# Performance work log

Measured on AMD Instinct MI355X. Metric: run time of the kernel, lower is better.

The kernel has to match this reference:

```python
import jax, jax.numpy as jnp
import numpy as np

B = 16384        # batch
I = 35           # input_dim (number of metadata features)
E = 256          # embedding_dim
C = E // 4       # continuous_size = 64


def setup_inputs() -> dict:
    key = jax.random.key(0)
    ks = jax.random.split(key, 12)
    # metadata rows 0-2 are continuous (depth, coverage, read_length); row 3 is runtype in {-2,-1,0,1}
    cont = jax.random.normal(ks[0], (B, 3, I), dtype=jnp.float32)
    run = jax.random.randint(ks[1], (B, 1, I), -2, 2).astype(jnp.float32)
    metadata = jnp.concatenate([cont, run], axis=1)  # [B, 4, I]
    s = 0.05
    return {
        "metadata": metadata,
        # per-feature Linear(1, C): weight [I, C] (squeezed from (C,1)), bias [I, C]
        "Wd": jax.random.normal(ks[2], (I, C), jnp.float32) * s,
        "bd": jax.random.normal(ks[3], (I, C), jnp.float32) * s,
        "Wc": jax.random.normal(ks[4], (I, C), jnp.float32) * s,
        "bc": jax.random.normal(ks[5], (I, C), jnp.float32) * s,
        "Wr": jax.random.normal(ks[6], (I, C), jnp.float32) * s,
        "br": jax.random.normal(ks[7], (I, C), jnp.float32) * s,
        # per-feature Embedding(4, C): [I, 4, C]
        "emb": jax.random.normal(ks[8], (I, 4, C), jnp.float32) * s,
        # final Linear(I*4*C -> E), torch convention weight [out, in]
        "Wf": jax.random.normal(ks[9], (E, I * 4 * C), jnp.float32) * s,
        "bf": jax.random.normal(ks[10], (E,), jnp.float32) * s,
        # LayerNorm affine params
        "gamma": jnp.ones((E,), jnp.float32),
        "beta": jnp.zeros((E,), jnp.float32),
    }


def _layer_norm(x, gamma, beta, eps=1e-5):
    mu = jnp.mean(x, axis=-1, keepdims=True)
    var = jnp.var(x, axis=-1, keepdims=True)  # biased, matches torch LayerNorm
    return (x - mu) * jax.lax.rsqrt(var + eps) * gamma + beta


def reference(metadata, Wd, bd, Wc, bc, Wr, br, emb, Wf, bf, gamma, beta):
    depth = metadata[:, 0, :]   # [B, I]
    cov = metadata[:, 1, :]
    rlen = metadata[:, 2, :]
    rt = metadata[:, 3, :].astype(jnp.int32)  # [B, I]
    rt = jnp.where(rt == -1, 2, rt)
    rt = jnp.where(rt == -2, 3, rt)

    # fused per-feature Linear(1, C): scalar * weight + bias, broadcast over all features at once
    de = depth[:, :, None] * Wd[None] + bd[None]   # [B, I, C]
    ce = cov[:, :, None] * Wc[None] + bc[None]     # [B, I, C]
    re_ = rlen[:, :, None] * Wr[None] + br[None]   # [B, I, C]
    # per-feature embedding gather: emb[i, rt[b, i]] -> [B, I, C]
    rte = emb[jnp.arange(I)[None, :], rt]

    feat = jnp.concatenate([de, ce, re_, rte], axis=-1)  # [B, I, 4C]
    feat = feat.reshape(B, I * 4 * C)                    # [B, 8960]

    out = feat @ Wf.T + bf                               # [B, E]
    out = _layer_norm(out, gamma, beta)
    return jnp.maximum(out, 0.0)  # non_linearity=True -> ReLU
```

## Files before the change

kernel.cpp:

```cpp
#include <hip/hip_runtime.h>

#define B_    16384
#define I_    35
#define ISLOT 36
#define E_    256
#define KP    288
#define F_    140
#define MROWS 32
#define NBLK  (B_ / MROWS)
#define LROW  296

typedef short bf16x8 __attribute__((ext_vector_type(8)));
typedef float f32x4  __attribute__((ext_vector_type(4)));

__device__ __forceinline__ unsigned short f2bf(float f) {
    unsigned int u = __float_as_uint(f);
    u += 0x7FFFu + ((u >> 16) & 1u);
    return (unsigned short)(u >> 16);
}

__global__ __launch_bounds__(256) void precompute_kernel(
    const float* __restrict__ Wd, const float* __restrict__ bd,
    const float* __restrict__ Wc, const float* __restrict__ bc,
    const float* __restrict__ Wr, const float* __restrict__ br,
    const float* __restrict__ emb, const float* __restrict__ Wf,
    const float* __restrict__ bf,
    unsigned short* __restrict__ At, float* __restrict__ base)
{
    __shared__ float wfs[8960];
    __shared__ float dots[7][40];
    __shared__ float bds[3][40];
    const int e = blockIdx.x, t = threadIdx.x;

    const float4* src = (const float4*)(Wf + (size_t)e * 8960);
    float4* dst = (float4*)wfs;
    for (int idx = t; idx < 2240; idx += 256) dst[idx] = src[idx];
    __syncthreads();

    if (t < 245) {
        const int g = t / 35, i = t - 35 * g;
        const int gsel = (g < 3) ? g : 3;
        const float* wf = wfs + i * 256 + gsel * 64;
        const float* tab = (g == 0) ? (Wd + i * 64)
                         : (g == 1) ? (Wc + i * 64)
                         : (g == 2) ? (Wr + i * 64)
                         : (emb + ((size_t)i * 4 + (g - 3)) * 64);
        const float* btab = (g == 0) ? (bd + i * 64)
                          : (g == 1) ? (bc + i * 64) : (br + i * 64);
        float dot = 0.f, bdot = 0.f;
        #pragma unroll 16
        for (int cc = 0; cc < 64; ++cc) {
            const int c = (cc + t) & 63;
            const float wv = wf[c];
            dot = fmaf(tab[c], wv, dot);
            if (g < 3) bdot = fmaf(btab[c], wv, bdot);
        }
        dots[g][i] = dot;
        if (g < 3) bds[g][i] = bdot;
    }
    __syncthreads();

    if (t < ISLOT) {
        union { unsigned short h[8]; int4 v; } p;
        if (t < I_) {
            const float v0 = dots[3][t], v1 = dots[4][t], v2 = dots[5][t], v3 = dots[6][t];
            const float a = v1 - v0, b = v2 - v0, c = v3 - v0;
            const float k2 = 0.5f * (a + b);
            const float s  = 0.5f * (a - b);
            const float u  = 0.5f * (4.f * k2 - c);
            const float k3 = (u - s) * (1.f / 3.f);
            const float k1 = s - k3;
            p.h[0] = f2bf(dots[0][t]); p.h[1] = f2bf(dots[1][t]); p.h[2] = f2bf(dots[2][t]);
            p.h[3] = f2bf(k1);         p.h[4] = f2bf(k2);         p.h[5] = f2bf(k3);
            p.h[6] = 0; p.h[7] = 0;
        } else {
            p.v = make_int4(0, 0, 0, 0);
        }
        *(int4*)(At + (size_t)e * KP + t * 8) = p.v;
    }
    if (t < 64) {
        float part = (t < I_) ? (bds[0][t] + bds[1][t] + bds[2][t] + dots[3][t]) : 0.f;
        #pragma unroll
        for (int mm = 1; mm < 64; mm <<= 1) part += __shfl_xor(part, mm, 64);
        if (t == 0) base[e] = bf[e] + part;
    }
}

__global__ __launch_bounds__(256) void main_kernel(
    const float* __restrict__ metadata,
    const unsigned short* __restrict__ At,
    const float* __restrict__ base,
    const float* __restrict__ gamma, const float* __restrict__ beta,
    float* __restrict__ out)
{
    __shared__ unsigned short feat[MROWS * LROW];
    __shared__ float redS[4][MROWS];
    __shared__ float redQ[4][MROWS];

    const int t  = threadIdx.x;
    const int b0 = blockIdx.x * MROWS;

    const int lane = t & 63, w = t >> 6;
    const int nlo = lane & 15, q = lane >> 4;

    float baseN[4], gmN[4], btN[4];
    #pragma unroll
    for (int nn = 0; nn < 4; ++nn) {
        const int e = w * 64 + nn * 16 + nlo;
        baseN[nn] = base[e]; gmN[nn] = gamma[e]; btN[nn] = beta[e];
    }

    for (int cell = t; cell < MROWS * ISLOT; cell += 256) {
        const int r = cell / ISLOT, i = cell - r * ISLOT;
        union { unsigned short h[8]; int4 v; } p;
        if (i < I_) {
            const float* mp = metadata + (size_t)(b0 + r) * F_ + i;
            const float d = mp[0], c = mp[I_], rl = mp[2 * I_], x = mp[3 * I_];
            const float x2 = x * x, x3 = x2 * x;
            p.h[0] = f2bf(d);  p.h[1] = f2bf(c);  p.h[2] = f2bf(rl);
            p.h[3] = f2bf(x);  p.h[4] = f2bf(x2); p.h[5] = f2bf(x3);
            p.h[6] = 0; p.h[7] = 0;
        } else {
            p.v = make_int4(0, 0, 0, 0);
        }
        *(int4*)(feat + r * LROW + i * 8) = p.v;
    }
    __syncthreads();

    f32x4 acc[2][4];
    #pragma unroll
    for (int mt = 0; mt < 2; ++mt)
        #pragma unroll
        for (int nn = 0; nn < 4; ++nn) acc[mt][nn] = (f32x4){0.f, 0.f, 0.f, 0.f};

    const unsigned short* ga = feat + nlo * LROW + q * 8;
    const unsigned short* gb = At + ((size_t)(w * 64 + nlo)) * KP + q * 8;

    #pragma unroll 3
    for (int ks = 0; ks < KP / 32; ++ks) {
        const bf16x8 a0 = *(const bf16x8*)(ga + ks * 32);
        const bf16x8 a1 = *(const bf16x8*)(ga + 16 * LROW + ks * 32);
        #pragma unroll
        for (int nn = 0; nn < 4; ++nn) {
            const bf16x8 b = *(const bf16x8*)(gb + (size_t)nn * 16 * KP + ks * 32);
            acc[0][nn] = __builtin_amdgcn_mfma_f32_16x16x32_bf16(a0, b, acc[0][nn], 0, 0, 0);
            acc[1][nn] = __builtin_amdgcn_mfma_f32_16x16x32_bf16(a1, b, acc[1][nn], 0, 0, 0);
        }
    }

    #pragma unroll
    for (int mt = 0; mt < 2; ++mt) {
        #pragma unroll
        for (int reg = 0; reg < 4; ++reg) {
            float s = 0.f, qq = 0.f;
            #pragma unroll
            for (int nn = 0; nn < 4; ++nn) {
                const float v = acc[mt][nn][reg] + baseN[nn];
                acc[mt][nn][reg] = v;
                s += v; qq += v * v;
            }
            #pragma unroll
            for (int mm = 1; mm < 16; mm <<= 1) {
                s  += __shfl_xor(s, mm, 64);
                qq += __shfl_xor(qq, mm, 64);
            }
            if (nlo == 0) {
                const int row = mt * 16 + q * 4 + reg;
                redS[w][row] = s; redQ[w][row] = qq;
            }
        }
    }
    __syncthreads();

    #pragma unroll
    for (int mt = 0; mt < 2; ++mt) {
        #pragma unroll
        for (int reg = 0; reg < 4; ++reg) {
            const int row = mt * 16 + q * 4 + reg;
            const float S = redS[0][row] + redS[1][row] + redS[2][row] + redS[3][row];
            const float Q = redQ[0][row] + redQ[1][row] + redQ[2][row] + redQ[3][row];
            const float mu   = S * (1.f / E_);
            const float var  = Q * (1.f / E_) - mu * mu;
            const float rstd = rsqrtf(var + 1e-5f);
            float* orow = out + (size_t)(b0 + row) * E_ + w * 64 + nlo;
            #pragma unroll
            for (int nn = 0; nn < 4; ++nn) {
                const float v = (acc[mt][nn][reg] - mu) * rstd * gmN[nn] + btN[nn];
                orow[nn * 16] = fmaxf(v, 0.f);
            }
        }
    }
}

extern "C" void kernel_launch(void* const* d_in, const int* in_sizes, int n_in,
                              void* d_out, int out_size, void* d_ws, size_t ws_size,
                              hipStream_t stream) {
    const float* metadata = (const float*)d_in[0];
    const float* Wd  = (const float*)d_in[1];
    const float* bd  = (const float*)d_in[2];
    const float* Wc  = (const float*)d_in[3];
    const float* bc  = (const float*)d_in[4];
    const float* Wr  = (const float*)d_in[5];
    const float* br  = (const float*)d_in[6];
    const float* emb = (const float*)d_in[7];
    const float* Wf  = (const float*)d_in[8];
    const float* bf  = (const float*)d_in[9];
    const float* gamma = (const float*)d_in[10];
    const float* beta  = (const float*)d_in[11];

    unsigned short* At = (unsigned short*)d_ws;
    float* basep = (float*)((char*)d_ws + (size_t)E_ * KP * 2);

    precompute_kernel<<<E_, 256, 0, stream>>>(Wd, bd, Wc, bc, Wr, br, emb, Wf, bf,
                                              At, basep);
    main_kernel<<<NBLK, 256, 0, stream>>>(metadata, At, basep, gamma, beta,
                                          (float*)d_out);
}
```

Baseline: 123.6 us.

## Pack K dimension densely, permute output columns for float4 stores, parallelize precompute

Measured after the change: 106.9 us, median of 2. -13.5%, faster.

```diff
diff --git a/kernel.cpp b/kernel.cpp
--- a/kernel.cpp
+++ b/kernel.cpp
@@ -2,13 +2,12 @@
 
 #define B_    16384
 #define I_    35
-#define ISLOT 36
 #define E_    256
-#define KP    288
+#define KP    224
 #define F_    140
 #define MROWS 32
 #define NBLK  (B_ / MROWS)
-#define LROW  296
+#define LROW  232
 
 typedef short bf16x8 __attribute__((ext_vector_type(8)));
 typedef float f32x4  __attribute__((ext_vector_type(4)));
@@ -19,7 +18,7 @@
     return (unsigned short)(u >> 16);
 }
 
-__global__ __launch_bounds__(256) void precompute_kernel(
+__global__ __launch_bounds__(512) void precompute_kernel(
     const float* __restrict__ Wd, const float* __restrict__ bd,
     const float* __restrict__ Wc, const float* __restrict__ bc,
     const float* __restrict__ Wr, const float* __restrict__ br,
@@ -27,56 +26,74 @@
     const float* __restrict__ bf,
     unsigned short* __restrict__ At, float* __restrict__ base)
 {
-    __shared__ float wfs[8960];
     __shared__ float dots[7][40];
     __shared__ float bds[3][40];
     const int e = blockIdx.x, t = threadIdx.x;
-
-    const float4* src = (const float4*)(Wf + (size_t)e * 8960);
-    float4* dst = (float4*)wfs;
-    for (int idx = t; idx < 2240; idx += 256) dst[idx] = src[idx];
+    const int grp = t >> 4, gl = t & 15;
+
+    const float* wfrow = Wf + (size_t)e * 8960;
+
+    for (int u = grp; u < 140; u += 32) {
+        const int i = u >> 2, part = u & 3;
+        const float* wf = wfrow + i * 256 + part * 64;
+        float wv[4];
+        #pragma unroll
+        for (int j = 0; j < 4; ++j) wv[j] = wf[gl + 16 * j];
+        if (part < 3) {
+            const float* tab  = ((part == 0) ? Wd : (part == 1) ? Wc : Wr) + i * 64;
+            const float* btab = ((part == 0) ? bd : (part == 1) ? bc : br) + i * 64;
+            float dot = 0.f, bdot = 0.f;
+            #pragma unroll
+            for (int j = 0; j < 4; ++j) {
+                const int c = gl + 16 * j;
+                dot  = fmaf(tab[c],  wv[j], dot);
+                bdot = fmaf(btab[c], wv[j], bdot);
+            }
+            #pragma unroll
+            for (int mm = 1; mm < 16; mm <<= 1) {
+                dot  += __shfl_xor(dot,  mm, 64);
+                bdot += __shfl_xor(bdot, mm, 64);
+            }
+            if (gl == 0) { dots[part][i] = dot; bds[part][i] = bdot; }
+        } else {
+            const float* et = emb + (size_t)i * 256;
+            float d0 = 0.f, d1 = 0.f, d2 = 0.f, d3 = 0.f;
+            #pragma unroll
+            for (int j = 0; j < 4; ++j) {
+                const int c = gl + 16 * j;
+                d0 = fmaf(et[c],       wv[j], d0);
+                d1 = fmaf(et[64 + c],  wv[j], d1);
+                d2 = fmaf(et[128 + c], wv[j], d2);
+                d3 = fmaf(et[192 + c], wv[j], d3);
+            }
+            #pragma unroll
+            for (int mm = 1; mm < 16; mm <<= 1) {
+                d0 += __shfl_xor(d0, mm, 64);
+                d1 += __shfl_xor(d1, mm, 64);
+                d2 += __shfl_xor(d2, mm, 64);
+                d3 += __shfl_xor(d3, mm, 64);
+            }
+            if (gl == 0) { dots[3][i] = d0; dots[4][i] = d1; dots[5][i] = d2; dots[6][i] = d3; }
+        }
+    }
     __syncthreads();
 
-    if (t < 245) {
-        const int g = t / 35, i = t - 35 * g;
-        const int gsel = (g < 3) ? g : 3;
-        const float* wf = wfs + i * 256 + gsel * 64;
-        const float* tab = (g == 0) ? (Wd + i * 64)
-                         : (g == 1) ? (Wc + i * 64)
-                         : (g == 2) ? (Wr + i * 64)
-                         : (emb + ((size_t)i * 4 + (g - 3)) * 64);
-        const float* btab = (g == 0) ? (bd + i * 64)
-                          : (g == 1) ? (bc + i * 64) : (br + i * 64);
-        float dot = 0.f, bdot = 0.f;
-        #pragma unroll 16
-        for (int cc = 0; cc < 64; ++cc) {
-            const int c = (cc + t) & 63;
-            const float wv = wf[c];
-            dot = fmaf(tab[c], wv, dot);
-            if (g < 3) bdot = fmaf(btab[c], wv, bdot);
-        }
-        dots[g][i] = dot;
-        if (g < 3) bds[g][i] = bdot;
-    }
-    __syncthreads();
-
-    if (t < ISLOT) {
-        union { unsigned short h[8]; int4 v; } p;
-        if (t < I_) {
-            const float v0 = dots[3][t], v1 = dots[4][t], v2 = dots[5][t], v3 = dots[6][t];
-            const float a = v1 - v0, b = v2 - v0, c = v3 - v0;
-            const float k2 = 0.5f * (a + b);
-            const float s  = 0.5f * (a - b);
-            const float u  = 0.5f * (4.f * k2 - c);
-            const float k3 = (u - s) * (1.f / 3.f);
-            const float k1 = s - k3;
-            p.h[0] = f2bf(dots[0][t]); p.h[1] = f2bf(dots[1][t]); p.h[2] = f2bf(dots[2][t]);
-            p.h[3] = f2bf(k1);         p.h[4] = f2bf(k2);         p.h[5] = f2bf(k3);
-            p.h[6] = 0; p.h[7] = 0;
-        } else {
-            p.v = make_int4(0, 0, 0, 0);
-        }
-        *(int4*)(At + (size_t)e * KP + t * 8) = p.v;
+    const int v = (e & ~63) | ((e & 3) << 4) | ((e & 63) >> 2);
+
+    if (t < I_) {
+        const float v0 = dots[3][t], v1 = dots[4][t], v2 = dots[5][t], v3 = dots[6][t];
+        const float a = v1 - v0, b = v2 - v0, c = v3 - v0;
+        const float k2 = 0.5f * (a + b);
+        const float s  = 0.5f * (a - b);
+        const float uu = 0.5f * (4.f * k2 - c);
+        const float k3 = (uu - s) * (1.f / 3.f);
+        const float k1 = s - k3;
+        unsigned int* dst = (unsigned int*)(At + (size_t)v * KP + t * 6);
+        dst[0] = (unsigned int)f2bf(dots[0][t]) | ((unsigned int)f2bf(dots[1][t]) << 16);
+        dst[1] = (unsigned int)f2bf(dots[2][t]) | ((unsigned int)f2bf(k1) << 16);
+        dst[2] = (unsigned int)f2bf(k2)         | ((unsigned int)f2bf(k3) << 16);
+    } else if (t < I_ + 7) {
+        ((unsigned int*)(At + (size_t)v * KP))[105 + t - I_] = 0;
     }
     if (t < 64) {
         float part = (t < I_) ? (bds[0][t] + bds[1][t] + bds[2][t] + dots[3][t]) : 0.f;
@@ -103,27 +120,26 @@
     const int lane = t & 63, w = t >> 6;
     const int nlo = lane & 15, q = lane >> 4;
 
-    float baseN[4], gmN[4], btN[4];
-    #pragma unroll
-    for (int nn = 0; nn < 4; ++nn) {
-        const int e = w * 64 + nn * 16 + nlo;
-        baseN[nn] = base[e]; gmN[nn] = gamma[e]; btN[nn] = beta[e];
-    }
-
-    for (int cell = t; cell < MROWS * ISLOT; cell += 256) {
-        const int r = cell / ISLOT, i = cell - r * ISLOT;
-        union { unsigned short h[8]; int4 v; } p;
-        if (i < I_) {
-            const float* mp = metadata + (size_t)(b0 + r) * F_ + i;
-            const float d = mp[0], c = mp[I_], rl = mp[2 * I_], x = mp[3 * I_];
-            const float x2 = x * x, x3 = x2 * x;
-            p.h[0] = f2bf(d);  p.h[1] = f2bf(c);  p.h[2] = f2bf(rl);
-            p.h[3] = f2bf(x);  p.h[4] = f2bf(x2); p.h[5] = f2bf(x3);
-            p.h[6] = 0; p.h[7] = 0;
-        } else {
-            p.v = make_int4(0, 0, 0, 0);
-        }
-        *(int4*)(feat + r * LROW + i * 8) = p.v;
+    const float4 bs4 = *(const float4*)(base  + w * 64 + nlo * 4);
+    const float4 gm4 = *(const float4*)(gamma + w * 64 + nlo * 4);
+    const float4 bt4 = *(const float4*)(beta  + w * 64 + nlo * 4);
+    const float bsv[4] = {bs4.x, bs4.y, bs4.z, bs4.w};
+    const float gmv[4] = {gm4.x, gm4.y, gm4.z, gm4.w};
+    const float btv[4] = {bt4.x, bt4.y, bt4.z, bt4.w};
+
+    for (int cell = t; cell < MROWS * I_; cell += 256) {
+        const int r = cell / I_, i = cell - r * I_;
+        const float* mp = metadata + (size_t)(b0 + r) * F_ + i;
+        const float d = mp[0], c = mp[I_], rl = mp[2 * I_], x = mp[3 * I_];
+        const float x2 = x * x, x3 = x2 * x;
+        unsigned int* dw = (unsigned int*)(feat + r * LROW + i * 6);
+        dw[0] = (unsigned int)f2bf(d)  | ((unsigned int)f2bf(c)  << 16);
+        dw[1] = (unsigned int)f2bf(rl) | ((unsigned int)f2bf(x)  << 16);
+        dw[2] = (unsigned int)f2bf(x2) | ((unsigned int)f2bf(x3) << 16);
+    }
+    for (int z = t; z < MROWS * 7; z += 256) {
+        const int r = z / 7, j = z - r * 7;
+        ((unsigned int*)(feat + r * LROW + 210))[j] = 0;
     }
     __syncthreads();
 
@@ -136,7 +152,7 @@
     const unsigned short* ga = feat + nlo * LROW + q * 8;
     const unsigned short* gb = At + ((size_t)(w * 64 + nlo)) * KP + q * 8;
 
-    #pragma unroll 3
+    #pragma unroll
     for (int ks = 0; ks < KP / 32; ++ks) {
         const bf16x8 a0 = *(const bf16x8*)(ga + ks * 32);
         const bf16x8 a1 = *(const bf16x8*)(ga + 16 * LROW + ks * 32);
@@ -155,9 +171,9 @@
             float s = 0.f, qq = 0.f;
             #pragma unroll
             for (int nn = 0; nn < 4; ++nn) {
-                const float v = acc[mt][nn][reg] + baseN[nn];
-                acc[mt][nn][reg] = v;
-                s += v; qq += v * v;
+                const float vv = acc[mt][nn][reg] + bsv[nn];
+                acc[mt][nn][reg] = vv;
+                s += vv; qq += vv * vv;
             }
             #pragma unroll
             for (int mm = 1; mm < 16; mm <<= 1) {
@@ -182,12 +198,12 @@
             const float mu   = S * (1.f / E_);
             const float var  = Q * (1.f / E_) - mu * mu;
             const float rstd = rsqrtf(var + 1e-5f);
-            float* orow = out + (size_t)(b0 + row) * E_ + w * 64 + nlo;
-            #pragma unroll
-            for (int nn = 0; nn < 4; ++nn) {
-                const float v = (acc[mt][nn][reg] - mu) * rstd * gmN[nn] + btN[nn];
-                orow[nn * 16] = fmaxf(v, 0.f);
-            }
+            float4 o;
+            o.x = fmaxf((acc[mt][0][reg] - mu) * rstd * gmv[0] + btv[0], 0.f);
+            o.y = fmaxf((acc[mt][1][reg] - mu) * rstd * gmv[1] + btv[1], 0.f);
+            o.z = fmaxf((acc[mt][2][reg] - mu) * rstd * gmv[2] + btv[2], 0.f);
+            o.w = fmaxf((acc[mt][3][reg] - mu) * rstd * gmv[3] + btv[3], 0.f);
+            *(float4*)(out + (size_t)(b0 + row) * E_ + w * 64 + nlo * 4) = o;
         }
     }
 }
@@ -211,7 +227,7 @@
     unsigned short* At = (unsigned short*)d_ws;
     float* basep = (float*)((char*)d_ws + (size_t)E_ * KP * 2);
 
-    precompute_kernel<<<E_, 256, 0, stream>>>(Wd, bd, Wc, bc, Wr, br, emb, Wf, bf,
+    precompute_kernel<<<E_, 512, 0, stream>>>(Wd, bd, Wc, bc, Wr, br, emb, Wf, bf,
                                               At, basep);
     main_kernel<<<NBLK, 256, 0, stream>>>(metadata, At, basep, gamma, beta,
                                           (float*)d_out);
```
